# Optimization experiments

Measured on AMD Instinct MI355X. Metric: run time of the kernel, lower is better.

## Reference

```python
import jax, jax.numpy as jnp
import numpy as np

B, T, D_IN = 32, 512, 1024
D_HID = 512
D_CODE = 1024
K = 256  # codebook size
COMMIT = 0.25
LAMBDA_MMD = 0.5
LN_EPS = 1e-5


def setup_inputs() -> dict:
    key = jax.random.key(0)
    ks = jax.random.split(key, 20)
    def w(k, shape, scale=0.02):
        return jax.random.normal(k, shape, dtype=jnp.float32) * scale
    inp = {
        "x": jax.random.normal(ks[0], (B, T, D_IN), dtype=jnp.float32),
        "prior": jax.random.normal(ks[1], (B, D_CODE), dtype=jnp.float32),
        # encoder: Linear(1024,512) -> LN(512) -> ReLU -> Linear(512,1024)
        "enc_W1": w(ks[2], (D_IN, D_HID)), "enc_b1": jnp.zeros((D_HID,), jnp.float32),
        "ln_g": jnp.ones((D_HID,), jnp.float32), "ln_b": jnp.zeros((D_HID,), jnp.float32),
        "enc_W2": w(ks[3], (D_HID, D_CODE)), "enc_b2": jnp.zeros((D_CODE,), jnp.float32),
        # codebook, init uniform(-1/K, 1/K) like the torch module
        "codebook": jax.random.uniform(ks[4], (K, D_CODE), jnp.float32, -1.0 / K, 1.0 / K),
        # projector: Linear(1024,512) -> ReLU -> Linear(512,1024)
        "proj_W1": w(ks[5], (D_CODE, D_HID)), "proj_b1": jnp.zeros((D_HID,), jnp.float32),
        "proj_W2": w(ks[6], (D_HID, D_CODE)), "proj_b2": jnp.zeros((D_CODE,), jnp.float32),
        # GRU(1024 -> 1024), torch gate order (r, z, n)
        "gru_Wih": w(ks[7], (D_CODE, 3 * D_CODE)), "gru_Whh": w(ks[8], (D_CODE, 3 * D_CODE)),
        "gru_bih": jnp.zeros((3 * D_CODE,), jnp.float32), "gru_bhh": jnp.zeros((3 * D_CODE,), jnp.float32),
        # head: Linear(1024, 1024)
        "head_W": w(ks[9], (D_CODE, D_IN)), "head_b": jnp.zeros((D_IN,), jnp.float32),
    }
    return inp


def _gaussian_kernel(a, b):
    # exp(-cdist(a,b)^2 / dim)
    d = a.shape[1]
    sq = (jnp.sum(a * a, 1, keepdims=True) + jnp.sum(b * b, 1)[None, :]
          - 2.0 * a @ b.T)
    sq = jnp.maximum(sq, 0.0)
    return jnp.exp(-sq / d)


def _gru(quantized, Wih, Whh, bih, bhh):
    # quantized: [B, T, D]; precompute input projections, scan over time
    gx = jnp.einsum("btd,de->bte", quantized, Wih) + bih  # [B,T,3D]
    gx = jnp.swapaxes(gx, 0, 1)  # [T,B,3D]
    h0 = jnp.zeros((quantized.shape[0], Whh.shape[0]), quantized.dtype)

    def step(h, gxt):
        gh = h @ Whh + bhh
        xr, xz, xn = jnp.split(gxt, 3, axis=-1)
        hr, hz, hn = jnp.split(gh, 3, axis=-1)
        r = jax.nn.sigmoid(xr + hr)
        z = jax.nn.sigmoid(xz + hz)
        n = jnp.tanh(xn + r * hn)
        h_new = (1.0 - z) * n + z * h
        return h_new, h_new

    _, hs = jax.lax.scan(step, h0, gx)  # [T,B,D]
    return jnp.swapaxes(hs, 0, 1)  # [B,T,D]


def reference(x, prior, enc_W1, enc_b1, ln_g, ln_b, enc_W2, enc_b2, codebook,
              proj_W1, proj_b1, proj_W2, proj_b2,
              gru_Wih, gru_Whh, gru_bih, gru_bhh, head_W, head_b):
    # ---- encoder ----
    h = x @ enc_W1 + enc_b1
    mu = jnp.mean(h, -1, keepdims=True)
    var = jnp.mean((h - mu) ** 2, -1, keepdims=True)
    h = (h - mu) * jax.lax.rsqrt(var + LN_EPS) * ln_g + ln_b
    h = jax.nn.relu(h)
    features = h @ enc_W2 + enc_b2  # [B,T,D_CODE]

    # ---- vector quantizer ----
    flat = features.reshape(-1, D_CODE)  # [B*T, D]
    dist = (jnp.sum(flat * flat, 1, keepdims=True) + jnp.sum(codebook * codebook, 1)
            - 2.0 * flat @ codebook.T)  # [B*T, K]
    idx = jnp.argmin(dist, axis=1)  # [B*T]
    quantized = codebook[idx].reshape(features.shape)
    e_latent = jnp.mean((jax.lax.stop_gradient(quantized) - features) ** 2)
    q_latent = jnp.mean((quantized - jax.lax.stop_gradient(features)) ** 2)
    vq_loss = q_latent + COMMIT * e_latent
    quantized = features + jax.lax.stop_gradient(quantized - features)  # straight-through

    # ---- projector + MMD ----
    p = jax.nn.relu(quantized @ proj_W1 + proj_b1)
    aligned = p @ proj_W2 + proj_b2  # [B,T,D]
    xm = jnp.mean(aligned, axis=1)  # [B,D]
    xx = _gaussian_kernel(xm, xm).mean()
    yy = _gaussian_kernel(prior, prior).mean()
    xy = _gaussian_kernel(xm, prior).mean()
    mmd = xx + yy - 2.0 * xy

    # ---- GRU decoder + head ----
    context = _gru(quantized, gru_Wih, gru_Whh, gru_bih, gru_bhh)
    recon = context @ head_W + head_b  # [B,T,D_IN]
    recon_loss = jnp.mean((recon - x) ** 2)

    total = recon_loss + vq_loss + LAMBDA_MMD * mmd
    return jnp.stack([recon_loss, vq_loss, mmd, total])
```

## Files before the change

### kernel.cpp

```cpp
#include <hip/hip_runtime.h>


typedef __attribute__((ext_vector_type(4))) float  f32x4;
typedef __attribute__((ext_vector_type(8))) short  s16x8;
typedef __attribute__((ext_vector_type(4))) short  s16x4;
typedef __attribute__((ext_vector_type(8))) __bf16 bf16x8;

__device__ __forceinline__ short f2bf(float f) {
  __bf16 h = (__bf16)f;
  return __builtin_bit_cast(short, h);
}
__device__ __forceinline__ float bf2f(short s) {
  return (float)__builtin_bit_cast(__bf16, s);
}
__device__ __forceinline__ f32x4 mfma16(s16x8 a, s16x8 b, f32x4 c) {
  return __builtin_amdgcn_mfma_f32_16x16x32_bf16(
      __builtin_bit_cast(bf16x8, a), __builtin_bit_cast(bf16x8, b), c, 0, 0, 0);
}

template<bool AF32, int EPI>
__global__ __launch_bounds__(256)
void gemm_k(const void* __restrict__ Ap, const float* __restrict__ Bp,
            const float* __restrict__ bias, void* __restrict__ Cp,
            const float* __restrict__ Xref, float* __restrict__ accum,
            int M, int N, int K)
{
  __shared__ short As[128][72];
  __shared__ short Bs[128][72];
  const int tid  = threadIdx.x;
  const long bm  = (long)blockIdx.x * 128;
  const long bn  = (long)blockIdx.y * 128;
  const int wave = tid >> 6, lane = tid & 63;
  const int wm = (wave >> 1) * 64, wn = (wave & 1) * 64;
  const int l16 = lane & 15, quad = lane >> 4;

  f32x4 acc[4][4];
#pragma unroll
  for (int i = 0; i < 4; ++i)
#pragma unroll
    for (int j = 0; j < 4; ++j) acc[i][j] = (f32x4){0.f, 0.f, 0.f, 0.f};

  const int atc = tid & 15, atr = tid >> 4;
  const int btc = tid & 31, btr = tid >> 5;

  for (int kt = 0; kt < K; kt += 64) {
#pragma unroll
    for (int p = 0; p < 8; ++p) {
      int r = p * 16 + atr;
      if (AF32) {
        const float* src = (const float*)Ap + (bm + r) * (long)K + kt + atc * 4;
        f32x4 v = *(const f32x4*)src;
        s16x4 s;
        s.x = f2bf(v.x); s.y = f2bf(v.y); s.z = f2bf(v.z); s.w = f2bf(v.w);
        *(s16x4*)&As[r][atc * 4] = s;
      } else {
        const short* src = (const short*)Ap + (bm + r) * (long)K + kt + atc * 4;
        *(s16x4*)&As[r][atc * 4] = *(const s16x4*)src;
      }
    }
#pragma unroll
    for (int p = 0; p < 8; ++p) {
      int kk = p * 8 + btr;
      const float* brow = Bp + (long)(kt + kk) * N + bn + btc;
#pragma unroll
      for (int j = 0; j < 4; ++j) Bs[btc + 32 * j][kk] = f2bf(brow[32 * j]);
    }
    __syncthreads();
#pragma unroll
    for (int kk = 0; kk < 64; kk += 32) {
      s16x8 af[4], bf[4];
#pragma unroll
      for (int i = 0; i < 4; ++i)
        af[i] = *(const s16x8*)&As[wm + i * 16 + l16][kk + quad * 8];
#pragma unroll
      for (int j = 0; j < 4; ++j)
        bf[j] = *(const s16x8*)&Bs[wn + j * 16 + l16][kk + quad * 8];
#pragma unroll
      for (int i = 0; i < 4; ++i)
#pragma unroll
        for (int j = 0; j < 4; ++j) acc[i][j] = mfma16(af[i], bf[j], acc[i][j]);
    }
    __syncthreads();
  }

  if (EPI == 3) {
    float ls = 0.f;
#pragma unroll
    for (int i = 0; i < 4; ++i)
#pragma unroll
      for (int j = 0; j < 4; ++j) {
        long col = bn + wn + j * 16 + l16;
        float bv = bias[col];
#pragma unroll
        for (int r = 0; r < 4; ++r) {
          long row = bm + wm + i * 16 + quad * 4 + r;
          float v = acc[i][j][r] + bv;
          float d = v - Xref[row * N + col];
          ls += d * d;
        }
      }
#pragma unroll
    for (int off = 32; off > 0; off >>= 1) ls += __shfl_xor(ls, off, 64);
    if (lane == 0) atomicAdd(accum, ls);
  } else {
#pragma unroll
    for (int i = 0; i < 4; ++i)
#pragma unroll
      for (int j = 0; j < 4; ++j) {
        long col = bn + wn + j * 16 + l16;
        float bv = bias[col];
#pragma unroll
        for (int r = 0; r < 4; ++r) {
          long row = bm + wm + i * 16 + quad * 4 + r;
          float v = acc[i][j][r] + bv;
          if (EPI == 2) v = fmaxf(v, 0.f);
          if (EPI == 0) ((float*)Cp)[row * N + col] = v;
          else          ((short*)Cp)[row * N + col] = f2bf(v);
        }
      }
  }
}

__global__ __launch_bounds__(256)
void ln_relu_k(const float* __restrict__ hp, const float* __restrict__ g,
               const float* __restrict__ b, short* __restrict__ out)
{
  const int wave = threadIdx.x >> 6, lane = threadIdx.x & 63;
  const long row = (long)blockIdx.x * 4 + wave;
  const float* hr = hp + row * 512;
  const int c0 = lane * 4, c1 = 256 + lane * 4;
  f32x4 v0 = *(const f32x4*)(hr + c0);
  f32x4 v1 = *(const f32x4*)(hr + c1);
  float s  = v0.x + v0.y + v0.z + v0.w + v1.x + v1.y + v1.z + v1.w;
  float ss = v0.x*v0.x + v0.y*v0.y + v0.z*v0.z + v0.w*v0.w
           + v1.x*v1.x + v1.y*v1.y + v1.z*v1.z + v1.w*v1.w;
#pragma unroll
  for (int off = 32; off > 0; off >>= 1) {
    s  += __shfl_xor(s, off, 64);
    ss += __shfl_xor(ss, off, 64);
  }
  float mu  = s * (1.f / 512.f);
  float var = ss * (1.f / 512.f) - mu * mu;
  float rs  = rsqrtf(var + 1e-5f);
  f32x4 g0 = *(const f32x4*)(g + c0), bb0 = *(const f32x4*)(b + c0);
  f32x4 g1 = *(const f32x4*)(g + c1), bb1 = *(const f32x4*)(b + c1);
  s16x4 o0, o1;
#pragma unroll
  for (int e = 0; e < 4; ++e) {
    o0[e] = f2bf(fmaxf((v0[e] - mu) * rs * g0[e] + bb0[e], 0.f));
    o1[e] = f2bf(fmaxf((v1[e] - mu) * rs * g1[e] + bb1[e], 0.f));
  }
  *(s16x4*)(out + row * 512 + c0) = o0;
  *(s16x4*)(out + row * 512 + c1) = o1;
}

__global__ __launch_bounds__(256)
void prep_cb_k(const float* __restrict__ cb, float* __restrict__ cbT,
               float* __restrict__ cbBias)
{
  __shared__ float red[256];
  const int r = blockIdx.x, tid = threadIdx.x;
  const float* row = cb + (long)r * 1024;
  float ss = 0.f;
  for (int c = tid; c < 1024; c += 256) {
    float v = row[c];
    cbT[(long)c * 256 + r] = v;
    ss += v * v;
  }
  red[tid] = ss; __syncthreads();
  for (int st = 128; st > 0; st >>= 1) {
    if (tid < st) red[tid] += red[tid + st];
    __syncthreads();
  }
  if (tid == 0) cbBias[r] = -0.5f * red[0];
}

__global__ __launch_bounds__(256)
void vq_k(const float* __restrict__ sc, const short* __restrict__ feat,
          int* __restrict__ idxp, float* __restrict__ e_acc)
{
  __shared__ float ep[4];
  const int wave = threadIdx.x >> 6, lane = threadIdx.x & 63;
  const long row = (long)blockIdx.x * 4 + wave;
  f32x4 s = *(const f32x4*)(sc + row * 256 + lane * 4);
  float best = s.x; int bi = lane * 4;
  if (s.y > best) { best = s.y; bi = lane * 4 + 1; }
  if (s.z > best) { best = s.z; bi = lane * 4 + 2; }
  if (s.w > best) { best = s.w; bi = lane * 4 + 3; }
#pragma unroll
  for (int off = 32; off > 0; off >>= 1) {
    float ov = __shfl_xor(best, off, 64);
    int   oi = __shfl_xor(bi, off, 64);
    if (ov > best || (ov == best && oi < bi)) { best = ov; bi = oi; }
  }
  const short* fr = feat + row * 1024;
  float sq = 0.f;
#pragma unroll
  for (int p = 0; p < 2; ++p) {
    s16x8 v = *(const s16x8*)(fr + p * 512 + lane * 8);
#pragma unroll
    for (int e = 0; e < 8; ++e) { float f = bf2f(v[e]); sq += f * f; }
  }
#pragma unroll
  for (int off = 32; off > 0; off >>= 1) sq += __shfl_xor(sq, off, 64);
  if (lane == 0) { idxp[row] = bi; ep[wave] = sq - 2.f * best; }
  __syncthreads();
  if (threadIdx.x == 0) atomicAdd(e_acc, ep[0] + ep[1] + ep[2] + ep[3]);
}

__global__ __launch_bounds__(256)
void hist_xm_k(const int* __restrict__ idxp, const float* __restrict__ AC,
               float* __restrict__ xm)
{
  __shared__ int   hist[256];
  __shared__ float hf[256];
  const int b = blockIdx.x, tid = threadIdx.x;
  hist[tid] = 0; __syncthreads();
  for (int t = tid; t < 512; t += 256) atomicAdd(&hist[idxp[b * 512 + t]], 1);
  __syncthreads();
  hf[tid] = (float)hist[tid] * (1.f / 512.f);
  __syncthreads();
  for (int d = tid; d < 1024; d += 256) {
    float a = 0.f;
    for (int k = 0; k < 256; ++k) a += hf[k] * AC[(long)k * 1024 + d];
    xm[(long)b * 1024 + d] = a;
  }
}

__global__ __launch_bounds__(1024)
void mmd_k(const float* __restrict__ xm, const float* __restrict__ prior,
           float* __restrict__ mmd_out)
{
  extern __shared__ float xs[];
  __shared__ float red[48];
  const int tid = threadIdx.x;
  for (int i = tid; i < 32 * 1024; i += 1024)
    xs[(i >> 10) * 1028 + (i & 1023)] = xm[i];
  __syncthreads();
  const int i = tid >> 5, j = tid & 31;
  const float* xi = xs + i * 1028;
  const float* xj = xs + j * 1028;
  const float* pi = prior + (long)i * 1024;
  const float* pj = prior + (long)j * 1024;
  float dxx = 0.f, dyy = 0.f, dxy = 0.f;
  for (int d = 0; d < 1024; d += 4) {
    f32x4 a = *(const f32x4*)(xi + d);
    f32x4 b = *(const f32x4*)(xj + d);
    f32x4 p = *(const f32x4*)(pi + d);
    f32x4 q = *(const f32x4*)(pj + d);
#pragma unroll
    for (int e = 0; e < 4; ++e) {
      float t1 = a[e] - b[e]; dxx += t1 * t1;
      float t2 = p[e] - q[e]; dyy += t2 * t2;
      float t3 = a[e] - q[e]; dxy += t3 * t3;
    }
  }
  float kxx = __expf(-dxx * (1.f / 1024.f));
  float kyy = __expf(-dyy * (1.f / 1024.f));
  float kxy = __expf(-dxy * (1.f / 1024.f));
  const int wv = tid >> 6, lane = tid & 63;
#pragma unroll
  for (int off = 32; off > 0; off >>= 1) {
    kxx += __shfl_xor(kxx, off, 64);
    kyy += __shfl_xor(kyy, off, 64);
    kxy += __shfl_xor(kxy, off, 64);
  }
  if (lane == 0) { red[wv] = kxx; red[16 + wv] = kyy; red[32 + wv] = kxy; }
  __syncthreads();
  if (tid == 0) {
    float sxx = 0.f, syy = 0.f, sxy = 0.f;
    for (int w = 0; w < 16; ++w) {
      sxx += red[w]; syy += red[16 + w]; sxy += red[32 + w];
    }
    mmd_out[0] = (sxx + syy - 2.f * sxy) * (1.f / 1024.f);
  }
}

__global__ __launch_bounds__(128)
void gru_k(const float* __restrict__ Whh, const float* __restrict__ bhh,
           const float* __restrict__ cgx, const int* __restrict__ idxp,
           short* __restrict__ hbuf, short* __restrict__ ctx,
           int* __restrict__ bar)
{
  extern __shared__ short Bsl[];
  const int tid = threadIdx.x, g = blockIdx.x;
  const int wave = tid >> 6, lane = tid & 63;
  const int l16 = lane & 15, quad = lane >> 4;

  for (int i = tid; i < 48 * 1024; i += 128) {
    int c = i % 48, k = i / 48;
    int gate = c >> 4, dl = c & 15;
    Bsl[c * 1032 + k] = f2bf(Whh[(long)k * 3072 + gate * 1024 + g * 16 + dl]);
  }
  const int dcol = g * 16 + l16;
  const float bhr = bhh[dcol], bhz = bhh[dcol + 1024], bhn = bhh[dcol + 2048];
  const short* arow = hbuf + (long)(wave * 16 + l16) * 1024 + quad * 8;
  const short* b0 = &Bsl[(long)l16 * 1032 + quad * 8];
  const short* b1 = b0 + 16 * 1032;
  const short* b2 = b0 + 32 * 1032;
  float hreg[4] = {0.f, 0.f, 0.f, 0.f};
  int brow[4];
#pragma unroll
  for (int r = 0; r < 4; ++r) brow[r] = wave * 16 + quad * 4 + r;
  __syncthreads();

  for (int t = 0; t < 512; ++t) {
    float xr[4], xz[4], xn[4];
#pragma unroll
    for (int r = 0; r < 4; ++r) {
      int code = idxp[brow[r] * 512 + t];
      const float* gp = cgx + (long)code * 3072 + dcol;
      xr[r] = gp[0]; xz[r] = gp[1024]; xn[r] = gp[2048];
    }
    f32x4 ar_ = {0.f,0.f,0.f,0.f}, az = ar_, an = ar_;
#pragma unroll 4
    for (int ks = 0; ks < 32; ++ks) {
      s16x8 a  = *(const s16x8*)(arow + ks * 32);
      s16x8 vr = *(const s16x8*)(b0 + ks * 32);
      s16x8 vz = *(const s16x8*)(b1 + ks * 32);
      s16x8 vn = *(const s16x8*)(b2 + ks * 32);
      ar_ = mfma16(a, vr, ar_);
      az  = mfma16(a, vz, az);
      an  = mfma16(a, vn, an);
    }
#pragma unroll
    for (int r = 0; r < 4; ++r) {
      float rr = 1.f / (1.f + __expf(-(xr[r] + ar_[r] + bhr)));
      float zz = 1.f / (1.f + __expf(-(xz[r] + az[r] + bhz)));
      float nn = tanhf(xn[r] + rr * (an[r] + bhn));
      float h  = (1.f - zz) * nn + zz * hreg[r];
      hreg[r] = h;
      short hb = f2bf(h);
      hbuf[(long)brow[r] * 1024 + dcol] = hb;
      ctx[((long)brow[r] * 512 + t) * 1024 + dcol] = hb;
    }
    __syncthreads();
    if (tid == 0) {
      int old = __hip_atomic_fetch_add(&bar[0], 1, __ATOMIC_ACQ_REL,
                                       __HIP_MEMORY_SCOPE_AGENT);
      if (old == 64 * (t + 1) - 1) {
        __hip_atomic_store(&bar[1], t + 1, __ATOMIC_RELEASE,
                           __HIP_MEMORY_SCOPE_AGENT);
      } else {
        while (__hip_atomic_load(&bar[1], __ATOMIC_RELAXED,
                                 __HIP_MEMORY_SCOPE_AGENT) < t + 1) {}
        (void)__hip_atomic_load(&bar[1], __ATOMIC_ACQUIRE,
                                __HIP_MEMORY_SCOPE_AGENT);
      }
    }
    __syncthreads();
  }
}

__global__ void fin_k(const float* __restrict__ scal, float* __restrict__ out)
{
  float recon = scal[3] * (1.f / 16777216.f);
  float vq    = 1.25f * scal[2] * (1.f / 16777216.f);
  float mmd   = scal[4];
  out[0] = recon;
  out[1] = vq;
  out[2] = mmd;
  out[3] = recon + vq + 0.5f * mmd;
}

extern "C" void kernel_launch(void* const* d_in, const int* in_sizes, int n_in,
                              void* d_out, int out_size, void* d_ws, size_t ws_size,
                              hipStream_t stream)
{
  const float* x     = (const float*)d_in[0];
  const float* prior = (const float*)d_in[1];
  const float* encW1 = (const float*)d_in[2];
  const float* encb1 = (const float*)d_in[3];
  const float* lng   = (const float*)d_in[4];
  const float* lnb   = (const float*)d_in[5];
  const float* encW2 = (const float*)d_in[6];
  const float* encb2 = (const float*)d_in[7];
  const float* cb    = (const float*)d_in[8];
  const float* pW1   = (const float*)d_in[9];
  const float* pb1   = (const float*)d_in[10];
  const float* pW2   = (const float*)d_in[11];
  const float* pb2   = (const float*)d_in[12];
  const float* Wih   = (const float*)d_in[13];
  const float* Whh   = (const float*)d_in[14];
  const float* bih   = (const float*)d_in[15];
  const float* bhh   = (const float*)d_in[16];
  const float* headW = (const float*)d_in[17];
  const float* headb = (const float*)d_in[18];

  char* ws = (char*)d_ws;
  if (ws_size < 89654528) return;
  float* h_pre  = (float*)(ws + 0);
  float* scores = h_pre;
  short* h1     = (short*)(ws + 33554432);
  short* feat   = (short*)(ws + 50331648);
  short* ctx    = feat;
  float* cgx    = (float*)(ws + 83886080);
  float* AC     = (float*)(ws + 87031808);
  float* cbT    = (float*)(ws + 88080384);
  short* ch     = (short*)(ws + 89128960);
  float* xm     = (float*)(ws + 89391104);
  int*   idxp   = (int*)  (ws + 89522176);
  short* hbuf   = (short*)(ws + 89587712);
  float* scal   = (float*)(ws + 89653248);
  int*   bar    = (int*)scal;
  float* e_acc  = scal + 2;
  float* r_acc  = scal + 3;
  float* mmdv   = scal + 4;
  float* cbBias = (float*)(ws + 89653504);

  hipMemsetAsync(ws + 89587712, 0, 65536 + 256, stream);

  dim3 blk(256);
  prep_cb_k<<<256, blk, 0, stream>>>(cb, cbT, cbBias);
  gemm_k<true, 0><<<dim3(128, 4), blk, 0, stream>>>(
      x, encW1, encb1, h_pre, nullptr, nullptr, 16384, 512, 1024);
  ln_relu_k<<<4096, blk, 0, stream>>>(h_pre, lng, lnb, h1);
  gemm_k<false, 1><<<dim3(128, 8), blk, 0, stream>>>(
      h1, encW2, encb2, feat, nullptr, nullptr, 16384, 1024, 512);
  gemm_k<false, 0><<<dim3(128, 2), blk, 0, stream>>>(
      feat, cbT, cbBias, scores, nullptr, nullptr, 16384, 256, 1024);
  vq_k<<<4096, blk, 0, stream>>>(scores, feat, idxp, e_acc);
  gemm_k<true, 2><<<dim3(2, 4), blk, 0, stream>>>(
      cb, pW1, pb1, ch, nullptr, nullptr, 256, 512, 1024);
  gemm_k<false, 0><<<dim3(2, 8), blk, 0, stream>>>(
      ch, pW2, pb2, AC, nullptr, nullptr, 256, 1024, 512);
  gemm_k<true, 0><<<dim3(2, 24), blk, 0, stream>>>(
      cb, Wih, bih, cgx, nullptr, nullptr, 256, 3072, 1024);
  hist_xm_k<<<32, blk, 0, stream>>>(idxp, AC, xm);
  mmd_k<<<1, 1024, 32 * 1028 * 4, stream>>>(xm, prior, mmdv);
  gru_k<<<64, 128, 48 * 1032 * 2, stream>>>(Whh, bhh, cgx, idxp, hbuf, ctx, bar);
  gemm_k<false, 3><<<dim3(128, 8), blk, 0, stream>>>(
      ctx, headW, headb, nullptr, x, r_acc, 16384, 1024, 1024);
  fin_k<<<1, 1, 0, stream>>>(scal, (float*)d_out);
}
```

Measured before the change: 5.884 ms.

## Replace GRU grid barrier with per-wave flags and double-buffered hidden state

The per-step global barrier in the persistent GRU kernel (atomic counter plus two block syncs) is replaced by per-wave step flags that every wave polls, and the hidden state is double-buffered so no second barrier is needed. Hidden-state reads use relaxed agent-scope atomic 64-bit loads, writes pack two bf16 values into 32-bit stores, and the next step's gate-input gathers are prefetched behind the current step's compute. tanh is computed from an exp formula. This is meant to cut the synchronisation latency on the serial 512-step critical path. It relies on s_waitcnt-based ordering instead of release semantics, which carries memory-ordering risk.

```diff
diff --git a/kernel.cpp b/kernel.cpp
--- a/kernel.cpp
+++ b/kernel.cpp
@@ -5,6 +5,8 @@
 typedef __attribute__((ext_vector_type(8))) short  s16x8;
 typedef __attribute__((ext_vector_type(4))) short  s16x4;
 typedef __attribute__((ext_vector_type(8))) __bf16 bf16x8;
+typedef unsigned long long u64;
+typedef unsigned int       u32;
 
 __device__ __forceinline__ short f2bf(float f) {
   __bf16 h = (__bf16)f;
@@ -16,6 +18,15 @@
 __device__ __forceinline__ f32x4 mfma16(s16x8 a, s16x8 b, f32x4 c) {
   return __builtin_amdgcn_mfma_f32_16x16x32_bf16(
       __builtin_bit_cast(bf16x8, a), __builtin_bit_cast(bf16x8, b), c, 0, 0, 0);
+}
+__device__ __forceinline__ void vm_drain() {
+  asm volatile("s_waitcnt vmcnt(0)" ::: "memory");
+}
+__device__ __forceinline__ u64 ld_uc64(const u64* p) {
+  return __hip_atomic_load(p, __ATOMIC_RELAXED, __HIP_MEMORY_SCOPE_AGENT);
+}
+__device__ __forceinline__ void st_uc32(u32* p, u32 v) {
+  __hip_atomic_store(p, v, __ATOMIC_RELAXED, __HIP_MEMORY_SCOPE_AGENT);
 }
 
 template<bool AF32, int EPI>
@@ -276,11 +287,11 @@
   }
 }
 
-__global__ __launch_bounds__(128)
+__global__ __launch_bounds__(128, 1)
 void gru_k(const float* __restrict__ Whh, const float* __restrict__ bhh,
            const float* __restrict__ cgx, const int* __restrict__ idxp,
-           short* __restrict__ hbuf, short* __restrict__ ctx,
-           int* __restrict__ bar)
+           u32* __restrict__ hbuf, u32* __restrict__ ctx,
+           int* __restrict__ flags)
 {
   extern __shared__ short Bsl[];
   const int tid = threadIdx.x, g = blockIdx.x;
@@ -294,61 +305,80 @@
   }
   const int dcol = g * 16 + l16;
   const float bhr = bhh[dcol], bhz = bhh[dcol + 1024], bhn = bhh[dcol + 2048];
-  const short* arow = hbuf + (long)(wave * 16 + l16) * 1024 + quad * 8;
-  const short* b0 = &Bsl[(long)l16 * 1032 + quad * 8];
+  const short* b0 = &Bsl[l16 * 1032 + quad * 8];
   const short* b1 = b0 + 16 * 1032;
   const short* b2 = b0 + 32 * 1032;
+  const int arowbase = (wave * 16 + l16) * 512 + quad * 4;
   float hreg[4] = {0.f, 0.f, 0.f, 0.f};
   int brow[4];
 #pragma unroll
   for (int r = 0; r < 4; ++r) brow[r] = wave * 16 + quad * 4 + r;
-  __syncthreads();
+  const int myflag = g * 2 + wave;
+  __syncthreads();
+
+  float xr[4], xz[4], xn[4];
+#pragma unroll
+  for (int r = 0; r < 4; ++r) {
+    int code = idxp[brow[r] * 512];
+    const float* gp = cgx + (long)code * 3072 + dcol;
+    xr[r] = gp[0]; xz[r] = gp[1024]; xn[r] = gp[2048];
+  }
 
   for (int t = 0; t < 512; ++t) {
-    float xr[4], xz[4], xn[4];
-#pragma unroll
-    for (int r = 0; r < 4; ++r) {
-      int code = idxp[brow[r] * 512 + t];
-      const float* gp = cgx + (long)code * 3072 + dcol;
-      xr[r] = gp[0]; xz[r] = gp[1024]; xn[r] = gp[2048];
-    }
+    if (t > 0) {
+      int a, b;
+      do {
+        a = __hip_atomic_load(&flags[lane],      __ATOMIC_RELAXED,
+                              __HIP_MEMORY_SCOPE_AGENT);
+        b = __hip_atomic_load(&flags[64 + lane], __ATOMIC_RELAXED,
+                              __HIP_MEMORY_SCOPE_AGENT);
+      } while (__any(a < t || b < t));
+    }
+    const u64* ap = (const u64*)(hbuf + ((t & 1) << 14) + arowbase);
     f32x4 ar_ = {0.f,0.f,0.f,0.f}, az = ar_, an = ar_;
-#pragma unroll 4
+#pragma unroll 8
     for (int ks = 0; ks < 32; ++ks) {
-      s16x8 a  = *(const s16x8*)(arow + ks * 32);
+      u64 q0 = ld_uc64(ap + ks * 8);
+      u64 q1 = ld_uc64(ap + ks * 8 + 1);
+      union { u64 q[2]; s16x8 v; } ua; ua.q[0] = q0; ua.q[1] = q1;
       s16x8 vr = *(const s16x8*)(b0 + ks * 32);
       s16x8 vz = *(const s16x8*)(b1 + ks * 32);
       s16x8 vn = *(const s16x8*)(b2 + ks * 32);
-      ar_ = mfma16(a, vr, ar_);
-      az  = mfma16(a, vz, az);
-      an  = mfma16(a, vn, an);
+      ar_ = mfma16(ua.v, vr, ar_);
+      az  = mfma16(ua.v, vz, az);
+      an  = mfma16(ua.v, vn, an);
     }
 #pragma unroll
     for (int r = 0; r < 4; ++r) {
       float rr = 1.f / (1.f + __expf(-(xr[r] + ar_[r] + bhr)));
       float zz = 1.f / (1.f + __expf(-(xz[r] + az[r] + bhz)));
-      float nn = tanhf(xn[r] + rr * (an[r] + bhn));
-      float h  = (1.f - zz) * nn + zz * hreg[r];
-      hreg[r] = h;
-      short hb = f2bf(h);
-      hbuf[(long)brow[r] * 1024 + dcol] = hb;
-      ctx[((long)brow[r] * 512 + t) * 1024 + dcol] = hb;
-    }
-    __syncthreads();
-    if (tid == 0) {
-      int old = __hip_atomic_fetch_add(&bar[0], 1, __ATOMIC_ACQ_REL,
-                                       __HIP_MEMORY_SCOPE_AGENT);
-      if (old == 64 * (t + 1) - 1) {
-        __hip_atomic_store(&bar[1], t + 1, __ATOMIC_RELEASE,
-                           __HIP_MEMORY_SCOPE_AGENT);
-      } else {
-        while (__hip_atomic_load(&bar[1], __ATOMIC_RELAXED,
-                                 __HIP_MEMORY_SCOPE_AGENT) < t + 1) {}
-        (void)__hip_atomic_load(&bar[1], __ATOMIC_ACQUIRE,
-                                __HIP_MEMORY_SCOPE_AGENT);
+      float u  = xn[r] + rr * (an[r] + bhn);
+      float e  = __expf(-2.f * u);
+      float nn = (1.f - e) / (1.f + e);
+      hreg[r]  = (1.f - zz) * nn + zz * hreg[r];
+    }
+    int tn = (t + 1 < 512) ? t + 1 : 0;
+#pragma unroll
+    for (int r = 0; r < 4; ++r) {
+      int code = idxp[brow[r] * 512 + tn];
+      const float* gp = cgx + (long)code * 3072 + dcol;
+      xr[r] = gp[0]; xz[r] = gp[1024]; xn[r] = gp[2048];
+    }
+    u32* hdst = hbuf + (((t + 1) & 1) << 14);
+#pragma unroll
+    for (int r = 0; r < 4; ++r) {
+      unsigned short hb = (unsigned short)f2bf(hreg[r]);
+      u32 other = (u32)__shfl_xor((int)hb, 1, 64) & 0xffffu;
+      if ((l16 & 1) == 0) {
+        u32 w = (u32)hb | (other << 16);
+        st_uc32(hdst + brow[r] * 512 + (dcol >> 1), w);
+        ctx[((long)brow[r] * 512 + t) * 512 + (dcol >> 1)] = w;
       }
     }
-    __syncthreads();
+    vm_drain();
+    if (lane == 0)
+      __hip_atomic_store(&flags[myflag], t + 1, __ATOMIC_RELAXED,
+                         __HIP_MEMORY_SCOPE_AGENT);
   }
 }
 
@@ -391,24 +421,24 @@
   if (ws_size < 89654528) return;
   float* h_pre  = (float*)(ws + 0);
   float* scores = h_pre;
+  u32*   hbuf   = (u32*)(ws + 0);
+  int*   flags  = (int*)(ws + 131072);
   short* h1     = (short*)(ws + 33554432);
   short* feat   = (short*)(ws + 50331648);
-  short* ctx    = feat;
+  u32*   ctx    = (u32*)feat;
   float* cgx    = (float*)(ws + 83886080);
   float* AC     = (float*)(ws + 87031808);
   float* cbT    = (float*)(ws + 88080384);
   short* ch     = (short*)(ws + 89128960);
   float* xm     = (float*)(ws + 89391104);
   int*   idxp   = (int*)  (ws + 89522176);
-  short* hbuf   = (short*)(ws + 89587712);
   float* scal   = (float*)(ws + 89653248);
-  int*   bar    = (int*)scal;
   float* e_acc  = scal + 2;
   float* r_acc  = scal + 3;
   float* mmdv   = scal + 4;
   float* cbBias = (float*)(ws + 89653504);
 
-  hipMemsetAsync(ws + 89587712, 0, 65536 + 256, stream);
+  hipMemsetAsync(scal, 0, 256, stream);
 
   dim3 blk(256);
   prep_cb_k<<<256, blk, 0, stream>>>(cb, cbT, cbBias);
@@ -420,6 +450,7 @@
   gemm_k<false, 0><<<dim3(128, 2), blk, 0, stream>>>(
       feat, cbT, cbBias, scores, nullptr, nullptr, 16384, 256, 1024);
   vq_k<<<4096, blk, 0, stream>>>(scores, feat, idxp, e_acc);
+  hipMemsetAsync(ws, 0, 131072 + 512, stream);
   gemm_k<true, 2><<<dim3(2, 4), blk, 0, stream>>>(
       cb, pW1, pb1, ch, nullptr, nullptr, 256, 512, 1024);
   gemm_k<false, 0><<<dim3(2, 8), blk, 0, stream>>>(
@@ -428,7 +459,7 @@
       cb, Wih, bih, cgx, nullptr, nullptr, 256, 3072, 1024);
   hist_xm_k<<<32, blk, 0, stream>>>(idxp, AC, xm);
   mmd_k<<<1, 1024, 32 * 1028 * 4, stream>>>(xm, prior, mmdv);
-  gru_k<<<64, 128, 48 * 1032 * 2, stream>>>(Whh, bhh, cgx, idxp, hbuf, ctx, bar);
+  gru_k<<<64, 128, 48 * 1032 * 2, stream>>>(Whh, bhh, cgx, idxp, hbuf, ctx, flags);
   gemm_k<false, 3><<<dim3(128, 8), blk, 0, stream>>>(
       ctx, headW, headb, nullptr, x, r_acc, 16384, 1024, 1024);
   fin_k<<<1, 1, 0, stream>>>(scal, (float*)d_out);
```

Result: faster. 5.740 ms (-2.4%).
